# Kernel tuning notes

Hardware: AMD Instinct MI355X
Metric: run time of the kernel (lower is better)

## Reference

```python
import jax, jax.numpy as jnp
import numpy as np

EPS = 1e-5
D_MODEL = 128; D_INNER = 256; D_STATE = 64; D_CONV = 4; NHEADS = 8; HEADDIM = 32
N_LAYERS = 4; PATCH = 16; IMG = 512; BATCH = 16
D_IN_PROJ = 2 * D_INNER + 2 * D_STATE + NHEADS  # 648
CONV_DIM = D_INNER + 2 * D_STATE               # 384


def _layernorm(x, g, b):
    m = jnp.mean(x, -1, keepdims=True)
    v = jnp.mean((x - m) ** 2, -1, keepdims=True)
    return (x - m) * jax.lax.rsqrt(v + EPS) * g + b


def _mamba2(x, in_w, conv_w, conv_b, dt_bias, A_log, D_skip, norm_w, out_w):
    # x: (b, l, d_model). Faithful to mamba-ssm Mamba2 (ngroups=1, rmsnorm gated, D skip).
    b, l, _ = x.shape
    zxbcdt = jnp.einsum('bld,ed->ble', x, in_w)            # (b,l,648)
    z = zxbcdt[..., :D_INNER]
    xBC = zxbcdt[..., D_INNER:D_INNER + CONV_DIM]
    dt = zxbcdt[..., -NHEADS:]
    # causal depthwise conv1d (kernel D_CONV) + SiLU
    xpad = jnp.pad(xBC, ((0, 0), (D_CONV - 1, 0), (0, 0)))
    xc = conv_b + sum(xpad[:, k:k + l, :] * conv_w[:, k] for k in range(D_CONV))
    xc = jax.nn.silu(xc)
    xs = xc[..., :D_INNER]
    B = xc[..., D_INNER:D_INNER + D_STATE]                 # (b,l,n)
    C = xc[..., -D_STATE:]                                 # (b,l,n)
    dt = jax.nn.softplus(dt + dt_bias)                     # (b,l,h)
    dA = jnp.exp(dt * (-jnp.exp(A_log)))                   # (b,l,h)
    xh = xs.reshape(b, l, NHEADS, HEADDIM)                 # (b,l,h,p)

    def step(hstate, t):
        dA_t, dt_t, B_t, x_t, C_t = t
        hstate = hstate * dA_t[:, :, None, None] + jnp.einsum('bh,bn,bhp->bhpn', dt_t, B_t, x_t)
        return hstate, jnp.einsum('bhpn,bn->bhp', hstate, C_t)

    h0 = jnp.zeros((b, NHEADS, HEADDIM, D_STATE), x.dtype)
    _, ys = jax.lax.scan(step, h0, (dA.swapaxes(0, 1), dt.swapaxes(0, 1), B.swapaxes(0, 1), xh.swapaxes(0, 1), C.swapaxes(0, 1)))
    y = ys.swapaxes(0, 1) + D_skip[None, None, :, None] * xh
    y = y.reshape(b, l, D_INNER)
    y = y * jax.nn.silu(z)                                 # gate
    y = y * jax.lax.rsqrt(jnp.mean(y * y, -1, keepdims=True) + EPS) * norm_w  # gated RMSNorm
    return jnp.einsum('ble,de->bld', y, out_w)


def _forward(x, patch_w, patch_b, pe_g, pe_b, in_w, conv_w, conv_b, dt_bias, A_log,
             D_skip, ssm_norm_w, out_w, ln_g, ln_b, fn_g, fn_b, attn_w1, attn_b1, attn_w2, attn_b2):
    b = x.shape[0]
    Hp = x.shape[2] // PATCH; Wp = x.shape[3] // PATCH
    # patch-embed conv (stride==kernel) as a reshape + einsum
    xp = x.reshape(b, 3, Hp, PATCH, Wp, PATCH)
    tok = jnp.einsum('bchpwq,dcpq->bhwd', xp, patch_w) + patch_b
    tok = tok.reshape(b, Hp * Wp, D_MODEL)
    tok = _layernorm(tok, pe_g, pe_b)
    for i in range(N_LAYERS):
        res = tok
        tok = _layernorm(tok, ln_g[i], ln_b[i])
        tok = _mamba2(tok, in_w[i], conv_w[i], conv_b[i], dt_bias[i], A_log[i],
                      D_skip[i], ssm_norm_w[i], out_w[i])
        tok = tok + res
    tok = _layernorm(tok, fn_g, fn_b)
    # attention pooling
    h1 = jnp.tanh(jnp.einsum('bld,hd->blh', tok, attn_w1) + attn_b1)
    scores = jnp.einsum('blh,oh->blo', h1, attn_w2) + attn_b2
    w = jax.nn.softmax(scores, axis=1)
    pooled = jnp.sum(w * tok, axis=1)
    nrm = jnp.maximum(jnp.sqrt(jnp.sum(pooled * pooled, -1, keepdims=True)), 1e-12)
    return pooled / nrm


def setup_inputs() -> dict:
    key = jax.random.key(0)
    ks = jax.random.split(key, 16)
    n = lambda k, shape, s=0.02: (jax.random.normal(k, shape) * s).astype(jnp.float32)
    return {
        'x': jax.random.normal(ks[0], (BATCH, 3, IMG, IMG), jnp.float32),
        'patch_w': n(ks[1], (D_MODEL, 3, PATCH, PATCH)),
        'patch_b': jnp.zeros((D_MODEL,), jnp.float32),
        'pe_g': jnp.ones((D_MODEL,), jnp.float32),
        'pe_b': jnp.zeros((D_MODEL,), jnp.float32),
        'in_w': n(ks[2], (N_LAYERS, D_IN_PROJ, D_MODEL)),
        'conv_w': n(ks[3], (N_LAYERS, CONV_DIM, D_CONV), 0.1),
        'conv_b': jnp.zeros((N_LAYERS, CONV_DIM), jnp.float32),
        'dt_bias': n(ks[4], (N_LAYERS, NHEADS), 0.5),
        'A_log': jnp.log(jax.random.uniform(ks[5], (N_LAYERS, NHEADS), jnp.float32, 1.0, 16.0)),
        'D_skip': jnp.ones((N_LAYERS, NHEADS), jnp.float32),
        'ssm_norm_w': jnp.ones((N_LAYERS, D_INNER), jnp.float32),
        'out_w': n(ks[6], (N_LAYERS, D_MODEL, D_INNER)),
        'ln_g': jnp.ones((N_LAYERS, D_MODEL), jnp.float32),
        'ln_b': jnp.zeros((N_LAYERS, D_MODEL), jnp.float32),
        'fn_g': jnp.ones((D_MODEL,), jnp.float32),
        'fn_b': jnp.zeros((D_MODEL,), jnp.float32),
        'attn_w1': n(ks[7], (D_MODEL // 2, D_MODEL), 0.05),
        'attn_b1': jnp.zeros((D_MODEL // 2,), jnp.float32),
        'attn_w2': n(ks[8], (1, D_MODEL // 2), 0.05),
        'attn_b2': jnp.zeros((1,), jnp.float32),
    }


def reference(x, patch_w, patch_b, pe_g, pe_b, in_w, conv_w, conv_b, dt_bias, A_log,
              D_skip, ssm_norm_w, out_w, ln_g, ln_b, fn_g, fn_b, attn_w1, attn_b1, attn_w2, attn_b2):
    return _forward(x, patch_w, patch_b, pe_g, pe_b, in_w, conv_w, conv_b, dt_bias, A_log,
                    D_skip, ssm_norm_w, out_w, ln_g, ln_b, fn_g, fn_b, attn_w1, attn_b1, attn_w2, attn_b2)
```

## Files before the change

### kernel.cpp

```cpp
#include <hip/hip_runtime.h>
#include <math.h>

#define EPS 1e-5f

constexpr int NB      = 16;
constexpr int L       = 1024;
constexpr int DM      = 128;
constexpr int DI      = 256;
constexpr int DS      = 64;
constexpr int NH      = 8;
constexpr int DPROJ   = 648;
constexpr int CDIM    = 384;
constexpr int EPAD    = 656;

typedef __attribute__((ext_vector_type(8))) short short8v;
typedef __attribute__((ext_vector_type(4))) short short4v;
typedef __attribute__((ext_vector_type(4))) float f32x4;
typedef unsigned short ushort_t;

__device__ __forceinline__ float silu_f(float x){ return x / (1.f + expf(-x)); }
__device__ __forceinline__ ushort_t f2bf(float f){
  union { float f; unsigned int u; } v; v.f = f;
  unsigned int r = v.u + 0x7FFF + ((v.u >> 16) & 1);
  return (ushort_t)(r >> 16);
}
__device__ __forceinline__ float bf2f(ushort_t u){
  union { float f; unsigned int u; } v; v.u = ((unsigned int)u) << 16;
  return v.f;
}
__device__ __forceinline__ short8v pack8(float4 a, float4 b){
  short8v v;
  v[0]=(short)f2bf(a.x); v[1]=(short)f2bf(a.y); v[2]=(short)f2bf(a.z); v[3]=(short)f2bf(a.w);
  v[4]=(short)f2bf(b.x); v[5]=(short)f2bf(b.y); v[6]=(short)f2bf(b.z); v[7]=(short)f2bf(b.w);
  return v;
}

__global__ __launch_bounds__(256) void k_cvt(const float* __restrict__ in_w,
    const float* __restrict__ ln_g, const float* __restrict__ ln_b,
    const float* __restrict__ out_w, const float* __restrict__ nw,
    const float* __restrict__ patch_w, const float* __restrict__ w1,
    ushort_t* __restrict__ inwb, ushort_t* __restrict__ owb,
    ushort_t* __restrict__ pwb, float* __restrict__ biasin,
    ushort_t* __restrict__ w1b){
  const int R1 = 4 * EPAD * 128, R2 = 4 * 128 * 256, R3 = 128 * 768, R4 = 4 * EPAD, R5 = 64 * 128;
  int i = blockIdx.x * 256 + threadIdx.x;
  if (i < R1) {
    int ly = i / (EPAD * 128), rem = i % (EPAD * 128), e = rem >> 7, d = rem & 127;
    float v = 0.f;
    if (e < DPROJ) v = in_w[((size_t)ly * DPROJ + e) * 128 + d] * ln_g[ly * 128 + d];
    inwb[i] = f2bf(v);
    return;
  }
  i -= R1;
  if (i < R2) {
    int ly = i >> 15, rem = i & 32767, e = rem & 255;
    owb[i] = f2bf(out_w[i] * nw[ly * 256 + e]);
    return;
  }
  i -= R2;
  if (i < R3) { pwb[i] = f2bf(patch_w[i]); return; }
  i -= R3;
  if (i < R4) {
    int ly = i / EPAD, e = i % EPAD;
    float s = 0.f;
    if (e < DPROJ) {
      const float* r = in_w + ((size_t)ly * DPROJ + e) * 128;
      const float* b = ln_b + ly * 128;
      for (int d = 0; d < 128; ++d) s += r[d] * b[d];
    }
    biasin[i] = s;
    return;
  }
  i -= R4;
  if (i < R5) w1b[i] = f2bf(w1[i]);
}

__global__ __launch_bounds__(256) void k_patch(const float* __restrict__ x,
    const ushort_t* __restrict__ pwb, const float* __restrict__ pb,
    const float* __restrict__ pg, const float* __restrict__ pbe,
    float* __restrict__ tok){
  __shared__ ushort_t Al[64 * 128];
  __shared__ ushort_t Bl[128 * 128];
  __shared__ float spb[128], spg[128], spe[128];
  const int m0 = blockIdx.x * 64;
  const int tid = threadIdx.x;
  char* Ab = (char*)Al; char* Bb = (char*)Bl;
  if (tid < 128) { spb[tid] = pb[tid]; spg[tid] = pg[tid]; spe[tid] = pbe[tid]; }
  const int w = tid >> 6, l = tid & 63, lr = l & 15, lgp = l >> 4;
  f32x4 acc[8];
#pragma unroll
  for (int nt = 0; nt < 8; ++nt) acc[nt] = (f32x4){0.f, 0.f, 0.f, 0.f};
  for (int kc = 0; kc < 6; ++kc) {
    __syncthreads();
    for (int idx = tid; idx < 128 * 16; idx += 256) {
      int n = idx >> 4, ch = idx & 15;
      short8v v = *(const short8v*)(pwb + (size_t)n * 768 + kc * 128 + (ch << 3));
      *(short8v*)(Bb + n * 256 + ((ch * 16) ^ ((n & 7) << 4))) = v;
    }
    {
      const int c = kc >> 1;
      for (int i = tid; i < 1024; i += 256) {
        int t = i >> 4, p = (i >> 1) & 7, o = i & 1;
        int T = m0 + t, bb = T >> 10, tl = T & 1023, hp = tl >> 5, wp = tl & 31;
        const float* src = x + (((size_t)(bb * 3 + c) * 512 + hp * 16 + ((kc & 1) << 3) + p) * 512
                                + wp * 16 + o * 8);
        float4 f0 = *(const float4*)src;
        float4 f1 = *(const float4*)(src + 4);
        short8v v = pack8(f0, f1);
        int kk = p * 16 + o * 8;
        *(short8v*)(Ab + t * 256 + ((kk * 2) ^ ((t & 7) << 4))) = v;
      }
    }
    __syncthreads();
    short8v a[4];
#pragma unroll
    for (int ks = 0; ks < 4; ++ks)
      a[ks] = *(const short8v*)(Ab + (16 * w + lr) * 256 + ((ks * 64 + lgp * 16) ^ ((lr & 7) << 4)));
#pragma unroll
    for (int nt = 0; nt < 8; ++nt) {
#pragma unroll
      for (int ks = 0; ks < 4; ++ks) {
        short8v b = *(const short8v*)(Bb + (nt * 16 + lr) * 256 + ((ks * 64 + lgp * 16) ^ ((lr & 7) << 4)));
        acc[nt] = __builtin_amdgcn_mfma_f32_16x16x32_bf16(a[ks], b, acc[nt], 0, 0, 0);
      }
    }
  }
  float s4[4] = {0,0,0,0}, q4[4] = {0,0,0,0};
#pragma unroll
  for (int nt = 0; nt < 8; ++nt) {
    const float bb = spb[nt * 16 + lr];
#pragma unroll
    for (int r = 0; r < 4; ++r) { float v = acc[nt][r] + bb; s4[r] += v; q4[r] += v * v; }
  }
#pragma unroll
  for (int r = 0; r < 4; ++r) {
    for (int off = 1; off < 16; off <<= 1) {
      s4[r] += __shfl_xor(s4[r], off, 16);
      q4[r] += __shfl_xor(q4[r], off, 16);
    }
  }
#pragma unroll
  for (int r = 0; r < 4; ++r) {
    float mean = s4[r] * (1.f / 128.f);
    float var  = q4[r] * (1.f / 128.f) - mean * mean;
    float rstd = rsqrtf(var + EPS);
    const size_t row = (size_t)(m0 + 16 * w + lgp * 4 + r) * 128;
#pragma unroll
    for (int nt = 0; nt < 8; ++nt) {
      int col = nt * 16 + lr;
      float v = acc[nt][r] + spb[col];
      tok[row + col] = (v - mean) * rstd * spg[col] + spe[col];
    }
  }
}

__global__ __launch_bounds__(256) void k_inproj(const float* __restrict__ tok,
    const ushort_t* __restrict__ inwb, const float* __restrict__ biasin,
    float* __restrict__ zx){
  __shared__ ushort_t Al[128 * 128];
  __shared__ ushort_t Bl[176 * 128];
  __shared__ float sBias[176];
  const int blk = blockIdx.x;
  const int mb = blk >> 2, nb = blk & 3;
  const int m0 = mb << 7, n0 = nb * 176;
  const int NT = (nb == 3) ? 128 : 176;
  const int tid = threadIdx.x;
  char* Ab = (char*)Al; char* Bb = (char*)Bl;
  for (int idx = tid; idx < (NT << 4); idx += 256) {
    int row = idx >> 4, ch = idx & 15;
    short8v v = *(const short8v*)(inwb + ((size_t)(n0 + row) << 7) + (ch << 3));
    *(short8v*)(Bb + row * 256 + ((ch * 16) ^ ((row & 7) << 4))) = v;
  }
  for (int idx = tid; idx < NT; idx += 256) sBias[idx] = biasin[n0 + idx];
  for (int rp = 0; rp < 2; ++rp) {
    const int r = (rp << 6) + (tid >> 2), t4 = tid & 3;
    const float* src = tok + (((size_t)(m0 + r)) << 7) + t4 * 32;
    float v[32];
    float s = 0.f, sq = 0.f;
#pragma unroll
    for (int k = 0; k < 8; ++k) {
      float4 f = *(const float4*)(src + 4 * k);
      v[4*k] = f.x; v[4*k+1] = f.y; v[4*k+2] = f.z; v[4*k+3] = f.w;
      s += f.x + f.y + f.z + f.w;
      sq += f.x*f.x + f.y*f.y + f.z*f.z + f.w*f.w;
    }
    s  += __shfl_xor(s, 1, 4);  s  += __shfl_xor(s, 2, 4);
    sq += __shfl_xor(sq, 1, 4); sq += __shfl_xor(sq, 2, 4);
    float mean = s * (1.f / 128.f);
    float var  = sq * (1.f / 128.f) - mean * mean;
    float rstd = rsqrtf(var + EPS);
#pragma unroll
    for (int k = 0; k < 4; ++k) {
      short8v o;
#pragma unroll
      for (int e = 0; e < 8; ++e) o[e] = (short)f2bf((v[8*k + e] - mean) * rstd);
      *(short8v*)(Ab + r * 256 + ((t4 * 64 + 16 * k) ^ ((r & 7) << 4))) = o;
    }
  }
  __syncthreads();
  const int w = tid >> 6, l = tid & 63, lr = l & 15, lgp = l >> 4;
  const int xsl = (lr & 7) << 4;
  short8v a[2][4];
#pragma unroll
  for (int mi = 0; mi < 2; ++mi) {
    const int mt = w + mi * 4;
#pragma unroll
    for (int ks = 0; ks < 4; ++ks)
      a[mi][ks] = *(const short8v*)(Ab + (16 * mt + lr) * 256 + ((ks * 64 + lgp * 16) ^ xsl));
  }
  const int NTT = NT >> 4;
  for (int nt = 0; nt < NTT; ++nt) {
    f32x4 acc0 = (f32x4){0.f, 0.f, 0.f, 0.f};
    f32x4 acc1 = (f32x4){0.f, 0.f, 0.f, 0.f};
#pragma unroll
    for (int ks = 0; ks < 4; ++ks) {
      short8v b = *(const short8v*)(Bb + (nt * 16 + lr) * 256 + ((ks * 64 + lgp * 16) ^ xsl));
      acc0 = __builtin_amdgcn_mfma_f32_16x16x32_bf16(a[0][ks], b, acc0, 0, 0, 0);
      acc1 = __builtin_amdgcn_mfma_f32_16x16x32_bf16(a[1][ks], b, acc1, 0, 0, 0);
    }
    const int col = n0 + nt * 16 + lr;
    if (col < DPROJ) {
      const float bias = sBias[nt * 16 + lr];
#pragma unroll
      for (int r = 0; r < 4; ++r) {
        zx[((size_t)(m0 + 16 * w       + lgp * 4 + r)) * DPROJ + col] = acc0[r] + bias;
        zx[((size_t)(m0 + 16 * (w + 4) + lgp * 4 + r)) * DPROJ + col] = acc1[r] + bias;
      }
    }
  }
}

constexpr int CONVC = 192;
__global__ __launch_bounds__(256) void k_conv(const float* __restrict__ zx,
    const float* __restrict__ cw, const float* __restrict__ cb,
    const float* __restrict__ dtbias, const float* __restrict__ Alog,
    ushort_t* __restrict__ xc, float* __restrict__ dtb,
    float* __restrict__ lcb, float* __restrict__ Acb){
  __shared__ float st[67][CONVC];
  __shared__ float swt[CONVC][4];
  __shared__ float sbias[CONVC];
  const int blk = blockIdx.x;
  const int cg = blk & 1, tile = (blk >> 1) & 15, b = blk >> 5;
  const int l0 = tile << 6, ch0 = cg * CONVC;
  const int tid = threadIdx.x;
  for (int i = tid; i < CONVC; i += 256) {
    float4 wv = *(const float4*)(cw + (size_t)(ch0 + i) * 4);
    swt[i][0] = wv.x; swt[i][1] = wv.y; swt[i][2] = wv.z; swt[i][3] = wv.w;
    sbias[i] = cb[ch0 + i];
  }
  for (int i = tid; i < 67 * 48; i += 256) {
    int rr = i / 48, q4 = i % 48;
    int lrow = l0 + rr - 3;
    float4 v = make_float4(0.f, 0.f, 0.f, 0.f);
    if (lrow >= 0) v = *(const float4*)(zx + ((size_t)(b << 10) + lrow) * DPROJ + DI + ch0 + q4 * 4);
    *(float4*)(&st[rr][q4 * 4]) = v;
  }
  if (cg == 0) {
    const int wv = tid >> 6, lane = tid & 63;
#pragma unroll
    for (int i = 0; i < 2; ++i) {
      const int hh = wv * 2 + i;
      float raw = zx[((size_t)(b << 10) + l0 + lane) * DPROJ + 640 + hh] + dtbias[hh];
      float dt = raw > 20.f ? raw : log1pf(expf(raw));
      float cum = dt * (-expf(Alog[hh]));
      for (int off = 1; off < 64; off <<= 1) {
        float v = __shfl_up(cum, off, 64);
        if (lane >= off) cum += v;
      }
      size_t o = ((size_t)((b << 3) + hh) << 10) + l0 + lane;
      dtb[o] = dt; lcb[o] = cum;
      if (lane == 63) Acb[((b << 3) + hh) * 16 + tile] = expf(cum);
    }
  }
  __syncthreads();
  for (int i = tid; i < 64 * 48; i += 256) {
    int t = i / 48, g = i % 48;
    short4v ov;
#pragma unroll
    for (int j = 0; j < 4; ++j) {
      int c2 = g * 4 + j;
      float acc = sbias[c2] + st[t][c2] * swt[c2][0] + st[t+1][c2] * swt[c2][1]
                + st[t+2][c2] * swt[c2][2] + st[t+3][c2] * swt[c2][3];
      ov[j] = (short)f2bf(silu_f(acc));
    }
    *(short4v*)(xc + ((size_t)(b << 10) + l0 + t) * CDIM + ch0 + g * 4) = ov;
  }
}

__global__ __launch_bounds__(256) void k_cstate(const ushort_t* __restrict__ xc,
    const float* __restrict__ dtb, const float* __restrict__ lcb,
    float* __restrict__ Sc){
  __shared__ ushort_t sXc[32 * 64];
  __shared__ ushort_t sBt[64 * 64];
  __shared__ float scoef[64];
  const int blk = blockIdx.x;
  const int c = blk & 15, h = (blk >> 4) & 7, b = blk >> 7;
  const int tid = threadIdx.x;
  const int l0 = c << 6;
  char* pA = (char*)sXc; char* pB = (char*)sBt;
  const size_t obh = ((size_t)((b << 3) + h) << 10) + l0;
  if (tid < 64) {
    float lcT = lcb[obh + 63];
    scoef[tid] = dtb[obh + tid] * __expf(fminf(lcT - lcb[obh + tid], 0.f));
  }
  const int s = tid >> 2, q = tid & 3;
  const ushort_t* xr = xc + ((size_t)(b << 10) + l0 + s) * CDIM;
  short8v b0 = *(const short8v*)(xr + 256 + q * 16);
  short8v b1 = *(const short8v*)(xr + 256 + q * 16 + 8);
  short8v x8 = *(const short8v*)(xr + (h << 5) + q * 8);
#pragma unroll
  for (int j = 0; j < 16; ++j) {
    const int n = q * 16 + j;
    ushort_t bv = (ushort_t)(j < 8 ? b0[j] : b1[j - 8]);
    *(ushort_t*)(pB + n * 128 + ((s * 2) ^ ((n & 7) << 4))) = bv;
  }
  __syncthreads();
  const float cf = scoef[s];
#pragma unroll
  for (int j = 0; j < 8; ++j) {
    const int p = q * 8 + j;
    *(ushort_t*)(pA + p * 128 + ((s * 2) ^ ((p & 7) << 4))) = f2bf(cf * bf2f((ushort_t)x8[j]));
  }
  __syncthreads();
  const int w = tid >> 6, l = tid & 63, lr = l & 15, lgp = l >> 4;
  const int xsl = (lr & 7) << 4;
  const int pt = w & 1, ng = w >> 1;
  short8v a0 = *(const short8v*)(pA + (pt * 16 + lr) * 128 + ((lgp * 16) ^ xsl));
  short8v a1 = *(const short8v*)(pA + (pt * 16 + lr) * 128 + ((64 + lgp * 16) ^ xsl));
  float* dst = Sc + ((size_t)blk << 11);
#pragma unroll
  for (int ni = 0; ni < 2; ++ni) {
    const int nt = ng * 2 + ni;
    f32x4 acc = (f32x4){0.f, 0.f, 0.f, 0.f};
    short8v bb0 = *(const short8v*)(pB + (nt * 16 + lr) * 128 + ((lgp * 16) ^ xsl));
    short8v bb1 = *(const short8v*)(pB + (nt * 16 + lr) * 128 + ((64 + lgp * 16) ^ xsl));
    acc = __builtin_amdgcn_mfma_f32_16x16x32_bf16(a0, bb0, acc, 0, 0, 0);
    acc = __builtin_amdgcn_mfma_f32_16x16x32_bf16(a1, bb1, acc, 0, 0, 0);
#pragma unroll
    for (int r = 0; r < 4; ++r)
      dst[(pt * 16 + lgp * 4 + r) * 64 + nt * 16 + lr] = acc[r];
  }
}

__global__ __launch_bounds__(256) void k_hscan(float* __restrict__ Sc, const float* __restrict__ Acb){
  const int blk = blockIdx.x;
  const int bh = blk >> 3;
  const int e = ((blk & 7) << 8) + threadIdx.x;
  float hs = 0.f;
  const size_t base = ((size_t)bh << 15) + e;
  for (int c = 0; c < 16; ++c) {
    const size_t o = base + ((size_t)c << 11);
    float v = Sc[o];
    Sc[o] = hs;
    hs = Acb[(bh << 4) + c] * hs + v;
  }
}

__global__ __launch_bounds__(256) void k_chunky(const ushort_t* __restrict__ xc,
    const float* __restrict__ h0buf, const float* __restrict__ dtb,
    const float* __restrict__ lcb, const float* __restrict__ Dsk,
    ushort_t* __restrict__ ys){
  __shared__ ushort_t sC[64 * 64];
  __shared__ ushort_t sBm[64 * 64];
  __shared__ ushort_t sAW[64 * 128];
  __shared__ ushort_t sBX[32 * 128];
  __shared__ float sXT[32][65];
  __shared__ float sdt[64], slc[64];
  const int blk = blockIdx.x;
  const int c = blk & 15, h = (blk >> 4) & 7, b = blk >> 7;
  const int tid = threadIdx.x;
  const int l0 = c << 6;
  char* pC = (char*)sC; char* pB = (char*)sBm; char* pA = (char*)sAW; char* pX = (char*)sBX;
  const size_t obh = ((size_t)((b << 3) + h) << 10) + l0;
  if (tid < 64) { sdt[tid] = dtb[obh + tid]; slc[tid] = lcb[obh + tid]; }
  {
    const int row = tid >> 2, q = tid & 3;
    const ushort_t* xr = xc + ((size_t)(b << 10) + l0 + row) * CDIM;
    const int xs = (row & 7) << 4;
    short8v b0 = *(const short8v*)(xr + 256 + q * 16);
    short8v b1 = *(const short8v*)(xr + 256 + q * 16 + 8);
    *(short8v*)(pB + row * 128 + ((q * 32) ^ xs))      = b0;
    *(short8v*)(pB + row * 128 + ((q * 32 + 16) ^ xs)) = b1;
    short8v c0 = *(const short8v*)(xr + 320 + q * 16);
    short8v c1 = *(const short8v*)(xr + 320 + q * 16 + 8);
    *(short8v*)(pC + row * 128 + ((q * 32) ^ xs))      = c0;
    *(short8v*)(pC + row * 128 + ((q * 32 + 16) ^ xs)) = c1;
    const float Pt = __expf(lcb[obh + row]);
    short8v q0, q1;
#pragma unroll
    for (int j = 0; j < 8; ++j) {
      q0[j] = (short)f2bf(Pt * bf2f((ushort_t)c0[j]));
      q1[j] = (short)f2bf(Pt * bf2f((ushort_t)c1[j]));
    }
    *(short8v*)(pA + row * 256 + ((128 + q * 32) ^ xs))      = q0;
    *(short8v*)(pA + row * 256 + ((128 + q * 32 + 16) ^ xs)) = q1;
    short8v x8 = *(const short8v*)(xr + (h << 5) + q * 8);
#pragma unroll
    for (int j = 0; j < 8; ++j) sXT[q * 8 + j][row] = bf2f((ushort_t)x8[j]);
  }
  {
    const int p = tid >> 3, n8 = (tid & 7) << 3;
    float4 h0a = *(const float4*)(h0buf + ((size_t)blk << 11) + (p << 6) + n8);
    float4 h0b = *(const float4*)(h0buf + ((size_t)blk << 11) + (p << 6) + n8 + 4);
    *(short8v*)(pX + p * 256 + (((64 + n8) * 2) ^ ((p & 7) << 4))) = pack8(h0a, h0b);
  }
  __syncthreads();
  {
    const int p = tid >> 3, s8 = (tid & 7) << 3;
    short8v vx;
#pragma unroll
    for (int e = 0; e < 8; ++e) vx[e] = (short)f2bf(sXT[p][s8 + e]);
    *(short8v*)(pX + p * 256 + ((s8 * 2) ^ ((p & 7) << 4))) = vx;
  }
  const int w = tid >> 6, l = tid & 63, lr = l & 15, lgp = l >> 4;
  const int xsl = (lr & 7) << 4;
  f32x4 accg[4];
#pragma unroll
  for (int nt = 0; nt < 4; ++nt) accg[nt] = (f32x4){0.f, 0.f, 0.f, 0.f};
  {
    short8v a0 = *(const short8v*)(pC + (16 * w + lr) * 128 + ((lgp * 16) ^ xsl));
    short8v a1 = *(const short8v*)(pC + (16 * w + lr) * 128 + ((64 + lgp * 16) ^ xsl));
#pragma unroll
    for (int nt = 0; nt < 4; ++nt) {
      short8v b0 = *(const short8v*)(pB + (nt * 16 + lr) * 128 + ((lgp * 16) ^ xsl));
      short8v b1 = *(const short8v*)(pB + (nt * 16 + lr) * 128 + ((64 + lgp * 16) ^ xsl));
      accg[nt] = __builtin_amdgcn_mfma_f32_16x16x32_bf16(a0, b0, accg[nt], 0, 0, 0);
      accg[nt] = __builtin_amdgcn_mfma_f32_16x16x32_bf16(a1, b1, accg[nt], 0, 0, 0);
    }
  }
#pragma unroll
  for (int nt = 0; nt < 4; ++nt) {
    const int s = nt * 16 + lr;
    const float ds = sdt[s], ls = slc[s];
#pragma unroll
    for (int r = 0; r < 4; ++r) {
      const int t = 16 * w + lgp * 4 + r;
      float wv = 0.f;
      if (s <= t) wv = ds * __expf(fminf(slc[t] - ls, 0.f)) * accg[nt][r];
      *(ushort_t*)(pA + t * 256 + ((s * 2) ^ ((t & 7) << 4))) = f2bf(wv);
    }
  }
  __syncthreads();
  f32x4 accy[2];
  accy[0] = (f32x4){0.f, 0.f, 0.f, 0.f};
  accy[1] = (f32x4){0.f, 0.f, 0.f, 0.f};
  short8v aw[4];
#pragma unroll
  for (int ks = 0; ks < 4; ++ks)
    aw[ks] = *(const short8v*)(pA + (16 * w + lr) * 256 + ((ks * 64 + lgp * 16) ^ xsl));
#pragma unroll
  for (int nt = 0; nt < 2; ++nt) {
#pragma unroll
    for (int ks = 0; ks < 4; ++ks) {
      short8v bx = *(const short8v*)(pX + (nt * 16 + lr) * 256 + ((ks * 64 + lgp * 16) ^ xsl));
      accy[nt] = __builtin_amdgcn_mfma_f32_16x16x32_bf16(aw[ks], bx, accy[nt], 0, 0, 0);
    }
  }
  const float dsk = Dsk[h];
#pragma unroll
  for (int nt = 0; nt < 2; ++nt) {
    const int p = nt * 16 + lr;
#pragma unroll
    for (int r = 0; r < 4; ++r) {
      const int t = 16 * w + lgp * 4 + r;
      ys[((size_t)(b << 10) + l0 + t) * DI + (h << 5) + p] = f2bf(accy[nt][r] + dsk * sXT[p][t]);
    }
  }
}

__global__ __launch_bounds__(256) void k_gateout(const float* __restrict__ zx,
    const ushort_t* __restrict__ ysb, const ushort_t* __restrict__ owb,
    float* __restrict__ tok){
  __shared__ ushort_t Al[64 * 256];
  __shared__ ushort_t Bl[128 * 64];
  const int m0 = blockIdx.x * 64;
  const int tid = threadIdx.x;
  char* Ab = (char*)Al; char* Bb = (char*)Bl;
  {
    const int r = tid >> 2, t4 = tid & 3;
    const size_t row = (size_t)(m0 + r);
    const ushort_t* yp = ysb + row * 256 + t4 * 64;
    const float* zp = zx + row * DPROJ + t4 * 64;
    float p[64];
    float sq = 0.f;
#pragma unroll
    for (int k = 0; k < 8; ++k) {
      short8v y8 = *(const short8v*)(yp + 8 * k);
      float4 fz0 = *(const float4*)(zp + 8 * k);
      float4 fz1 = *(const float4*)(zp + 8 * k + 4);
      float zz[8] = {fz0.x, fz0.y, fz0.z, fz0.w, fz1.x, fz1.y, fz1.z, fz1.w};
#pragma unroll
      for (int j = 0; j < 8; ++j) {
        float a = bf2f((ushort_t)y8[j]) * (zz[j] / (1.f + __expf(-zz[j])));
        p[8 * k + j] = a; sq += a * a;
      }
    }
    sq += __shfl_xor(sq, 1, 4); sq += __shfl_xor(sq, 2, 4);
    float rstd = rsqrtf(sq * (1.f / 256.f) + EPS);
#pragma unroll
    for (int k = 0; k < 8; ++k) {
      short8v o;
#pragma unroll
      for (int e = 0; e < 8; ++e) o[e] = (short)f2bf(p[8*k + e] * rstd);
      *(short8v*)(Ab + r * 512 + ((t4 * 128 + 16 * k) ^ ((r & 7) << 4))) = o;
    }
  }
  const int w = tid >> 6, l = tid & 63, lr = l & 15, lgp = l >> 4;
  f32x4 acc[8];
#pragma unroll
  for (int nt = 0; nt < 8; ++nt) acc[nt] = (f32x4){0.f, 0.f, 0.f, 0.f};
  for (int kq = 0; kq < 4; ++kq) {
    __syncthreads();
    for (int idx = tid; idx < 128 * 8; idx += 256) {
      int row = idx >> 3, ch = idx & 7;
      short8v v = *(const short8v*)(owb + ((size_t)row << 8) + kq * 64 + (ch << 3));
      *(short8v*)(Bb + row * 128 + ((ch * 16) ^ ((row & 7) << 4))) = v;
    }
    __syncthreads();
    short8v a0 = *(const short8v*)(Ab + (16*w + lr) * 512 + ((kq * 128 +      lgp * 16) ^ ((lr & 7) << 4)));
    short8v a1 = *(const short8v*)(Ab + (16*w + lr) * 512 + ((kq * 128 + 64 + lgp * 16) ^ ((lr & 7) << 4)));
#pragma unroll
    for (int nt = 0; nt < 8; ++nt) {
      short8v b0 = *(const short8v*)(Bb + (nt * 16 + lr) * 128 + ((     lgp * 16) ^ ((lr & 7) << 4)));
      short8v b1 = *(const short8v*)(Bb + (nt * 16 + lr) * 128 + ((64 + lgp * 16) ^ ((lr & 7) << 4)));
      acc[nt] = __builtin_amdgcn_mfma_f32_16x16x32_bf16(a0, b0, acc[nt], 0, 0, 0);
      acc[nt] = __builtin_amdgcn_mfma_f32_16x16x32_bf16(a1, b1, acc[nt], 0, 0, 0);
    }
  }
#pragma unroll
  for (int nt = 0; nt < 8; ++nt) {
#pragma unroll
    for (int r = 0; r < 4; ++r) {
      tok[((size_t)(m0 + 16 * w + lgp * 4 + r)) * 128 + nt * 16 + lr] += acc[nt][r];
    }
  }
}

__global__ __launch_bounds__(256) void k_score(const float* __restrict__ tok,
    const float* __restrict__ fg, const float* __restrict__ fb,
    const ushort_t* __restrict__ w1b, const float* __restrict__ b1,
    const float* __restrict__ w2, const float* __restrict__ b2,
    float* __restrict__ tokF, float* __restrict__ sc){
  __shared__ ushort_t Al[64 * 128];
  __shared__ ushort_t Wl[64 * 128];
  __shared__ float sb1[64], sw2[64];
  const int m0 = blockIdx.x * 64;
  const int tid = threadIdx.x;
  char* Ab = (char*)Al; char* Wb = (char*)Wl;
  for (int idx = tid; idx < 64 * 16; idx += 256) {
    int row = idx >> 4, ch = idx & 15;
    short8v v = *(const short8v*)(w1b + (row << 7) + (ch << 3));
    *(short8v*)(Wb + row * 256 + ((ch * 16) ^ ((row & 7) << 4))) = v;
  }
  if (tid < 64) { sb1[tid] = b1[tid]; sw2[tid] = w2[tid]; }
  {
    const int r = tid >> 2, t4 = tid & 3;
    const float* src = tok + (((size_t)(m0 + r)) << 7) + t4 * 32;
    float v[32];
    float s = 0.f, sq = 0.f;
#pragma unroll
    for (int k = 0; k < 8; ++k) {
      float4 f = *(const float4*)(src + 4 * k);
      v[4*k] = f.x; v[4*k+1] = f.y; v[4*k+2] = f.z; v[4*k+3] = f.w;
      s += f.x + f.y + f.z + f.w;
      sq += f.x*f.x + f.y*f.y + f.z*f.z + f.w*f.w;
    }
    s  += __shfl_xor(s, 1, 4);  s  += __shfl_xor(s, 2, 4);
    sq += __shfl_xor(sq, 1, 4); sq += __shfl_xor(sq, 2, 4);
    float mean = s * (1.f / 128.f);
    float var  = sq * (1.f / 128.f) - mean * mean;
    float rstd = rsqrtf(var + EPS);
    float* tdst = tokF + (((size_t)(m0 + r)) << 7) + t4 * 32;
#pragma unroll
    for (int k = 0; k < 4; ++k) {
      float o8[8];
      float4 g0 = *(const float4*)(fg + t4 * 32 + 8 * k);
      float4 g1 = *(const float4*)(fg + t4 * 32 + 8 * k + 4);
      float4 e0 = *(const float4*)(fb + t4 * 32 + 8 * k);
      float4 e1 = *(const float4*)(fb + t4 * 32 + 8 * k + 4);
      o8[0] = (v[8*k+0]-mean)*rstd*g0.x + e0.x; o8[1] = (v[8*k+1]-mean)*rstd*g0.y + e0.y;
      o8[2] = (v[8*k+2]-mean)*rstd*g0.z + e0.z; o8[3] = (v[8*k+3]-mean)*rstd*g0.w + e0.w;
      o8[4] = (v[8*k+4]-mean)*rstd*g1.x + e1.x; o8[5] = (v[8*k+5]-mean)*rstd*g1.y + e1.y;
      o8[6] = (v[8*k+6]-mean)*rstd*g1.z + e1.z; o8[7] = (v[8*k+7]-mean)*rstd*g1.w + e1.w;
      *(float4*)(tdst + 8*k)     = make_float4(o8[0], o8[1], o8[2], o8[3]);
      *(float4*)(tdst + 8*k + 4) = make_float4(o8[4], o8[5], o8[6], o8[7]);
      short8v ov;
#pragma unroll
      for (int e = 0; e < 8; ++e) ov[e] = (short)f2bf(o8[e]);
      *(short8v*)(Ab + r * 256 + ((t4 * 64 + 16 * k) ^ ((r & 7) << 4))) = ov;
    }
  }
  __syncthreads();
  const int w = tid >> 6, l = tid & 63, lr = l & 15, lgp = l >> 4;
  const int xsl = (lr & 7) << 4;
  short8v a[4];
#pragma unroll
  for (int ks = 0; ks < 4; ++ks)
    a[ks] = *(const short8v*)(Ab + (16 * w + lr) * 256 + ((ks * 64 + lgp * 16) ^ xsl));
  float sacc[4] = {0.f, 0.f, 0.f, 0.f};
#pragma unroll
  for (int nt = 0; nt < 4; ++nt) {
    f32x4 acc = (f32x4){0.f, 0.f, 0.f, 0.f};
#pragma unroll
    for (int ks = 0; ks < 4; ++ks) {
      short8v bb = *(const short8v*)(Wb + (nt * 16 + lr) * 256 + ((ks * 64 + lgp * 16) ^ xsl));
      acc = __builtin_amdgcn_mfma_f32_16x16x32_bf16(a[ks], bb, acc, 0, 0, 0);
    }
    const float bias = sb1[nt * 16 + lr], wv = sw2[nt * 16 + lr];
#pragma unroll
    for (int r = 0; r < 4; ++r) sacc[r] += tanhf(acc[r] + bias) * wv;
  }
#pragma unroll
  for (int r = 0; r < 4; ++r) {
    for (int off = 1; off < 16; off <<= 1) sacc[r] += __shfl_xor(sacc[r], off, 16);
  }
  if (lr == 0) {
    const float bb2 = b2[0];
#pragma unroll
    for (int r = 0; r < 4; ++r) sc[m0 + 16 * w + lgp * 4 + r] = sacc[r] + bb2;
  }
}

__global__ __launch_bounds__(256) void k_pool1(const float* __restrict__ tokF,
    const float* __restrict__ sc, float* __restrict__ pp){
  __shared__ float sw[128];
  __shared__ float sacc[128];
  __shared__ float sse[2];
  const int bs = blockIdx.x, b = bs >> 3, seg = bs & 7, tid = threadIdx.x;
  const int l0 = (b << 10) + (seg << 7);
  if (tid < 128) sw[tid] = __expf(sc[l0 + tid]);
  __syncthreads();
  const int d = tid & 127, g = tid >> 7;
  const float* tf = tokF + ((size_t)(l0 + (g << 6))) * 128 + d;
  float acc = 0.f;
#pragma unroll 4
  for (int i = 0; i < 64; ++i) acc += sw[(g << 6) + i] * tf[(size_t)i * 128];
  if (g == 0) sacc[d] = acc;
  float e = (tid < 128) ? sw[tid] : 0.f;
  for (int off = 32; off; off >>= 1) e += __shfl_xor(e, off);
  if ((tid & 63) == 0 && tid < 128) sse[tid >> 6] = e;
  __syncthreads();
  if (g == 1) pp[bs * 132 + d] = sacc[d] + acc;
  if (tid == 0) pp[bs * 132 + 128] = sse[0] + sse[1];
}

__global__ __launch_bounds__(128) void k_pool2(const float* __restrict__ pp,
    float* __restrict__ out){
  __shared__ float s2[2];
  const int b = blockIdx.x, tid = threadIdx.x;
  float num = 0.f, den = 0.f;
#pragma unroll
  for (int seg = 0; seg < 8; ++seg) {
    num += pp[(b * 8 + seg) * 132 + tid];
    den += pp[(b * 8 + seg) * 132 + 128];
  }
  float pooled = num / den;
  float sq = pooled * pooled;
  for (int off = 32; off; off >>= 1) sq += __shfl_xor(sq, off);
  if ((tid & 63) == 0) s2[tid >> 6] = sq;
  __syncthreads();
  float nrm = fmaxf(sqrtf(s2[0] + s2[1]), 1e-12f);
  out[(size_t)b * 128 + tid] = pooled / nrm;
}

extern "C" void kernel_launch(void* const* d_in, const int* in_sizes, int n_in,
                              void* d_out, int out_size, void* d_ws, size_t ws_size,
                              hipStream_t stream) {
  const float* x       = (const float*)d_in[0];
  const float* patch_w = (const float*)d_in[1];
  const float* patch_b = (const float*)d_in[2];
  const float* pe_g    = (const float*)d_in[3];
  const float* pe_b    = (const float*)d_in[4];
  const float* in_w    = (const float*)d_in[5];
  const float* conv_w  = (const float*)d_in[6];
  const float* conv_b  = (const float*)d_in[7];
  const float* dt_bias = (const float*)d_in[8];
  const float* A_log   = (const float*)d_in[9];
  const float* D_skip  = (const float*)d_in[10];
  const float* nw      = (const float*)d_in[11];
  const float* out_w   = (const float*)d_in[12];
  const float* ln_g    = (const float*)d_in[13];
  const float* ln_b    = (const float*)d_in[14];
  const float* fn_g    = (const float*)d_in[15];
  const float* fn_b    = (const float*)d_in[16];
  const float* w1      = (const float*)d_in[17];
  const float* b1      = (const float*)d_in[18];
  const float* w2      = (const float*)d_in[19];
  const float* b2      = (const float*)d_in[20];
  float* out = (float*)d_out;
  char* ws = (char*)d_ws;

  size_t off = 0;
  float* tok  = (float*)(ws + off); off += (size_t)NB * L * DM * 4;
  float* zx   = (float*)(ws + off); off += (size_t)NB * L * DPROJ * 4;
  ushort_t* xcb = (ushort_t*)(ws + off); off += (size_t)NB * L * CDIM * 2;
  ushort_t* ysb = (ushort_t*)(ws + off); off += (size_t)NB * L * DI * 2;
  float* Scb  = (float*)(ws + off); off += (size_t)NB * NH * 16 * 2048 * 4;
  float* dtb  = (float*)(ws + off); off += (size_t)NB * NH * L * 4;
  float* lcb  = (float*)(ws + off); off += (size_t)NB * NH * L * 4;
  float* Acb  = (float*)(ws + off); off += (size_t)NB * NH * 16 * 4;
  ushort_t* inwb = (ushort_t*)(ws + off); off += (size_t)4 * EPAD * 128 * 2;
  ushort_t* owb  = (ushort_t*)(ws + off); off += (size_t)4 * 128 * 256 * 2;
  ushort_t* pwb  = (ushort_t*)(ws + off); off += (size_t)128 * 768 * 2;
  float* biasin  = (float*)(ws + off); off += (size_t)4 * EPAD * 4;
  ushort_t* w1b  = (ushort_t*)(ws + off); off += (size_t)64 * 128 * 2;
  float* pp      = (float*)(ws + off); off += (size_t)128 * 132 * 4;
  float* tokF = zx;
  float* scb  = (float*)(ws + (size_t)30 * 1024 * 1024);

  {
    const int total = 4 * EPAD * 128 + 4 * 128 * 256 + 128 * 768 + 4 * EPAD + 64 * 128;
    k_cvt<<<(total + 255) / 256, 256, 0, stream>>>(in_w, ln_g, ln_b, out_w, nw, patch_w, w1,
                                                   inwb, owb, pwb, biasin, w1b);
  }
  k_patch<<<256, 256, 0, stream>>>(x, pwb, patch_b, pe_g, pe_b, tok);
  for (int ly = 0; ly < 4; ++ly) {
    k_inproj<<<512, 256, 0, stream>>>(tok, inwb + (size_t)ly * EPAD * 128,
                                      biasin + ly * EPAD, zx);
    k_conv<<<NB * 16 * 2, 256, 0, stream>>>(zx, conv_w + (size_t)ly * CDIM * 4,
                                            conv_b + ly * CDIM, dt_bias + ly * NH,
                                            A_log + ly * NH, xcb, dtb, lcb, Acb);
    k_cstate<<<NB * NH * 16, 256, 0, stream>>>(xcb, dtb, lcb, Scb);
    k_hscan<<<NB * NH * 8, 256, 0, stream>>>(Scb, Acb);
    k_chunky<<<NB * NH * 16, 256, 0, stream>>>(xcb, Scb, dtb, lcb,
                                               D_skip + ly * NH, ysb);
    k_gateout<<<256, 256, 0, stream>>>(zx, ysb, owb + (size_t)ly * 128 * 256, tok);
  }
  k_score<<<256, 256, 0, stream>>>(tok, fn_g, fn_b, w1b, b1, w2, b2, tokF, scb);
  k_pool1<<<128, 256, 0, stream>>>(tokF, scb, pp);
  k_pool2<<<16, 128, 0, stream>>>(pp, out);
}
```

Baseline: 478.5 us.

## Store in-proj output and chunk states in bf16, prefetch out-proj weights

Switches the large zx intermediate (in-projection output) and the per-chunk SSM state buffer from fp32 to bf16. This halves global memory traffic across inproj, conv, hscan, chunky and gateout. In gateout, the out-projection weight tiles are now prefetched into registers and staged through double-buffered shared memory, which removes one barrier per k-step. The cost is lower precision, including in the inter-chunk state recurrence that hscan runs in bf16 storage. The tokF and scb workspace offsets are moved to fit the new layout.

After: 430.1 us. 1.11x faster.

```diff
diff --git a/kernel.cpp b/kernel.cpp
--- a/kernel.cpp
+++ b/kernel.cpp
@@ -156,7 +156,7 @@
 
 __global__ __launch_bounds__(256) void k_inproj(const float* __restrict__ tok,
     const ushort_t* __restrict__ inwb, const float* __restrict__ biasin,
-    float* __restrict__ zx){
+    ushort_t* __restrict__ zxb){
   __shared__ ushort_t Al[128 * 128];
   __shared__ ushort_t Bl[176 * 128];
   __shared__ float sBias[176];
@@ -223,15 +223,15 @@
       const float bias = sBias[nt * 16 + lr];
 #pragma unroll
       for (int r = 0; r < 4; ++r) {
-        zx[((size_t)(m0 + 16 * w       + lgp * 4 + r)) * DPROJ + col] = acc0[r] + bias;
-        zx[((size_t)(m0 + 16 * (w + 4) + lgp * 4 + r)) * DPROJ + col] = acc1[r] + bias;
+        zxb[((size_t)(m0 + 16 * w       + lgp * 4 + r)) * DPROJ + col] = f2bf(acc0[r] + bias);
+        zxb[((size_t)(m0 + 16 * (w + 4) + lgp * 4 + r)) * DPROJ + col] = f2bf(acc1[r] + bias);
       }
     }
   }
 }
 
 constexpr int CONVC = 192;
-__global__ __launch_bounds__(256) void k_conv(const float* __restrict__ zx,
+__global__ __launch_bounds__(256) void k_conv(const ushort_t* __restrict__ zxb,
     const float* __restrict__ cw, const float* __restrict__ cb,
     const float* __restrict__ dtbias, const float* __restrict__ Alog,
     ushort_t* __restrict__ xc, float* __restrict__ dtb,
@@ -248,19 +248,24 @@
     swt[i][0] = wv.x; swt[i][1] = wv.y; swt[i][2] = wv.z; swt[i][3] = wv.w;
     sbias[i] = cb[ch0 + i];
   }
-  for (int i = tid; i < 67 * 48; i += 256) {
-    int rr = i / 48, q4 = i % 48;
+  for (int i = tid; i < 67 * 24; i += 256) {
+    int rr = i / 24, g = i % 24;
     int lrow = l0 + rr - 3;
-    float4 v = make_float4(0.f, 0.f, 0.f, 0.f);
-    if (lrow >= 0) v = *(const float4*)(zx + ((size_t)(b << 10) + lrow) * DPROJ + DI + ch0 + q4 * 4);
-    *(float4*)(&st[rr][q4 * 4]) = v;
+    float v[8] = {0,0,0,0,0,0,0,0};
+    if (lrow >= 0) {
+      short8v z8 = *(const short8v*)(zxb + ((size_t)(b << 10) + lrow) * DPROJ + DI + ch0 + g * 8);
+#pragma unroll
+      for (int j = 0; j < 8; ++j) v[j] = bf2f((ushort_t)z8[j]);
+    }
+    *(float4*)(&st[rr][g * 8])     = make_float4(v[0], v[1], v[2], v[3]);
+    *(float4*)(&st[rr][g * 8 + 4]) = make_float4(v[4], v[5], v[6], v[7]);
   }
   if (cg == 0) {
     const int wv = tid >> 6, lane = tid & 63;
 #pragma unroll
     for (int i = 0; i < 2; ++i) {
       const int hh = wv * 2 + i;
-      float raw = zx[((size_t)(b << 10) + l0 + lane) * DPROJ + 640 + hh] + dtbias[hh];
+      float raw = bf2f(zxb[((size_t)(b << 10) + l0 + lane) * DPROJ + 640 + hh]) + dtbias[hh];
       float dt = raw > 20.f ? raw : log1pf(expf(raw));
       float cum = dt * (-expf(Alog[hh]));
       for (int off = 1; off < 64; off <<= 1) {
@@ -289,7 +294,7 @@
 
 __global__ __launch_bounds__(256) void k_cstate(const ushort_t* __restrict__ xc,
     const float* __restrict__ dtb, const float* __restrict__ lcb,
-    float* __restrict__ Sc){
+    ushort_t* __restrict__ Sc){
   __shared__ ushort_t sXc[32 * 64];
   __shared__ ushort_t sBt[64 * 64];
   __shared__ float scoef[64];
@@ -327,7 +332,7 @@
   const int pt = w & 1, ng = w >> 1;
   short8v a0 = *(const short8v*)(pA + (pt * 16 + lr) * 128 + ((lgp * 16) ^ xsl));
   short8v a1 = *(const short8v*)(pA + (pt * 16 + lr) * 128 + ((64 + lgp * 16) ^ xsl));
-  float* dst = Sc + ((size_t)blk << 11);
+  ushort_t* dst = Sc + ((size_t)blk << 11);
 #pragma unroll
   for (int ni = 0; ni < 2; ++ni) {
     const int nt = ng * 2 + ni;
@@ -338,11 +343,11 @@
     acc = __builtin_amdgcn_mfma_f32_16x16x32_bf16(a1, bb1, acc, 0, 0, 0);
 #pragma unroll
     for (int r = 0; r < 4; ++r)
-      dst[(pt * 16 + lgp * 4 + r) * 64 + nt * 16 + lr] = acc[r];
-  }
-}
-
-__global__ __launch_bounds__(256) void k_hscan(float* __restrict__ Sc, const float* __restrict__ Acb){
+      dst[(pt * 16 + lgp * 4 + r) * 64 + nt * 16 + lr] = f2bf(acc[r]);
+  }
+}
+
+__global__ __launch_bounds__(256) void k_hscan(ushort_t* __restrict__ Sc, const float* __restrict__ Acb){
   const int blk = blockIdx.x;
   const int bh = blk >> 3;
   const int e = ((blk & 7) << 8) + threadIdx.x;
@@ -350,14 +355,14 @@
   const size_t base = ((size_t)bh << 15) + e;
   for (int c = 0; c < 16; ++c) {
     const size_t o = base + ((size_t)c << 11);
-    float v = Sc[o];
-    Sc[o] = hs;
+    float v = bf2f(Sc[o]);
+    Sc[o] = f2bf(hs);
     hs = Acb[(bh << 4) + c] * hs + v;
   }
 }
 
 __global__ __launch_bounds__(256) void k_chunky(const ushort_t* __restrict__ xc,
-    const float* __restrict__ h0buf, const float* __restrict__ dtb,
+    const ushort_t* __restrict__ h0buf, const float* __restrict__ dtb,
     const float* __restrict__ lcb, const float* __restrict__ Dsk,
     ushort_t* __restrict__ ys){
   __shared__ ushort_t sC[64 * 64];
@@ -400,9 +405,8 @@
   }
   {
     const int p = tid >> 3, n8 = (tid & 7) << 3;
-    float4 h0a = *(const float4*)(h0buf + ((size_t)blk << 11) + (p << 6) + n8);
-    float4 h0b = *(const float4*)(h0buf + ((size_t)blk << 11) + (p << 6) + n8 + 4);
-    *(short8v*)(pX + p * 256 + (((64 + n8) * 2) ^ ((p & 7) << 4))) = pack8(h0a, h0b);
+    short8v h8 = *(const short8v*)(h0buf + ((size_t)blk << 11) + (p << 6) + n8);
+    *(short8v*)(pX + p * 256 + (((64 + n8) * 2) ^ ((p & 7) << 4))) = h8;
   }
   __syncthreads();
   {
@@ -468,30 +472,29 @@
   }
 }
 
-__global__ __launch_bounds__(256) void k_gateout(const float* __restrict__ zx,
+__global__ __launch_bounds__(256) void k_gateout(const ushort_t* __restrict__ zxb,
     const ushort_t* __restrict__ ysb, const ushort_t* __restrict__ owb,
     float* __restrict__ tok){
   __shared__ ushort_t Al[64 * 256];
-  __shared__ ushort_t Bl[128 * 64];
+  __shared__ ushort_t Bl[2][128 * 64];
   const int m0 = blockIdx.x * 64;
   const int tid = threadIdx.x;
-  char* Ab = (char*)Al; char* Bb = (char*)Bl;
+  char* Ab = (char*)Al;
   {
     const int r = tid >> 2, t4 = tid & 3;
     const size_t row = (size_t)(m0 + r);
     const ushort_t* yp = ysb + row * 256 + t4 * 64;
-    const float* zp = zx + row * DPROJ + t4 * 64;
+    const ushort_t* zp = zxb + row * DPROJ + t4 * 64;
     float p[64];
     float sq = 0.f;
 #pragma unroll
     for (int k = 0; k < 8; ++k) {
       short8v y8 = *(const short8v*)(yp + 8 * k);
-      float4 fz0 = *(const float4*)(zp + 8 * k);
-      float4 fz1 = *(const float4*)(zp + 8 * k + 4);
-      float zz[8] = {fz0.x, fz0.y, fz0.z, fz0.w, fz1.x, fz1.y, fz1.z, fz1.w};
+      short8v z8 = *(const short8v*)(zp + 8 * k);
 #pragma unroll
       for (int j = 0; j < 8; ++j) {
-        float a = bf2f((ushort_t)y8[j]) * (zz[j] / (1.f + __expf(-zz[j])));
+        float zz = bf2f((ushort_t)z8[j]);
+        float a = bf2f((ushort_t)y8[j]) * (zz / (1.f + __expf(-zz)));
         p[8 * k + j] = a; sq += a * a;
       }
     }
@@ -505,18 +508,32 @@
       *(short8v*)(Ab + r * 512 + ((t4 * 128 + 16 * k) ^ ((r & 7) << 4))) = o;
     }
   }
+  short8v breg[4];
+#pragma unroll
+  for (int j = 0; j < 4; ++j) {
+    int idx = tid + 256 * j, row = idx >> 3, ch = idx & 7;
+    breg[j] = *(const short8v*)(owb + ((size_t)row << 8) + (ch << 3));
+  }
   const int w = tid >> 6, l = tid & 63, lr = l & 15, lgp = l >> 4;
   f32x4 acc[8];
 #pragma unroll
   for (int nt = 0; nt < 8; ++nt) acc[nt] = (f32x4){0.f, 0.f, 0.f, 0.f};
+  int buf = 0;
   for (int kq = 0; kq < 4; ++kq) {
+    char* Bb = (char*)Bl[buf];
+#pragma unroll
+    for (int j = 0; j < 4; ++j) {
+      int idx = tid + 256 * j, row = idx >> 3, ch = idx & 7;
+      *(short8v*)(Bb + row * 128 + ((ch * 16) ^ ((row & 7) << 4))) = breg[j];
+    }
     __syncthreads();
-    for (int idx = tid; idx < 128 * 8; idx += 256) {
-      int row = idx >> 3, ch = idx & 7;
-      short8v v = *(const short8v*)(owb + ((size_t)row << 8) + kq * 64 + (ch << 3));
-      *(short8v*)(Bb + row * 128 + ((ch * 16) ^ ((row & 7) << 4))) = v;
-    }
-    __syncthreads();
+    if (kq < 3) {
+#pragma unroll
+      for (int j = 0; j < 4; ++j) {
+        int idx = tid + 256 * j, row = idx >> 3, ch = idx & 7;
+        breg[j] = *(const short8v*)(owb + ((size_t)row << 8) + (kq + 1) * 64 + (ch << 3));
+      }
+    }
     short8v a0 = *(const short8v*)(Ab + (16*w + lr) * 512 + ((kq * 128 +      lgp * 16) ^ ((lr & 7) << 4)));
     short8v a1 = *(const short8v*)(Ab + (16*w + lr) * 512 + ((kq * 128 + 64 + lgp * 16) ^ ((lr & 7) << 4)));
 #pragma unroll
@@ -526,6 +543,7 @@
       acc[nt] = __builtin_amdgcn_mfma_f32_16x16x32_bf16(a0, b0, acc[nt], 0, 0, 0);
       acc[nt] = __builtin_amdgcn_mfma_f32_16x16x32_bf16(a1, b1, acc[nt], 0, 0, 0);
     }
+    buf ^= 1;
   }
 #pragma unroll
   for (int nt = 0; nt < 8; ++nt) {
@@ -692,10 +710,10 @@
 
   size_t off = 0;
   float* tok  = (float*)(ws + off); off += (size_t)NB * L * DM * 4;
-  float* zx   = (float*)(ws + off); off += (size_t)NB * L * DPROJ * 4;
+  ushort_t* zxb = (ushort_t*)(ws + off); off += (size_t)NB * L * DPROJ * 2;
   ushort_t* xcb = (ushort_t*)(ws + off); off += (size_t)NB * L * CDIM * 2;
   ushort_t* ysb = (ushort_t*)(ws + off); off += (size_t)NB * L * DI * 2;
-  float* Scb  = (float*)(ws + off); off += (size_t)NB * NH * 16 * 2048 * 4;
+  ushort_t* Scb = (ushort_t*)(ws + off); off += (size_t)NB * NH * 16 * 2048 * 2;
   float* dtb  = (float*)(ws + off); off += (size_t)NB * NH * L * 4;
   float* lcb  = (float*)(ws + off); off += (size_t)NB * NH * L * 4;
   float* Acb  = (float*)(ws + off); off += (size_t)NB * NH * 16 * 4;
@@ -705,8 +723,8 @@
   float* biasin  = (float*)(ws + off); off += (size_t)4 * EPAD * 4;
   ushort_t* w1b  = (ushort_t*)(ws + off); off += (size_t)64 * 128 * 2;
   float* pp      = (float*)(ws + off); off += (size_t)128 * 132 * 4;
-  float* tokF = zx;
-  float* scb  = (float*)(ws + (size_t)30 * 1024 * 1024);
+  float* tokF = (float*)(ws + (size_t)8 * 1024 * 1024);
+  float* scb  = (float*)(ws + (size_t)17 * 1024 * 1024);
 
   {
     const int total = 4 * EPAD * 128 + 4 * 128 * 256 + 128 * 768 + 4 * EPAD + 64 * 128;
@@ -716,15 +734,15 @@
   k_patch<<<256, 256, 0, stream>>>(x, pwb, patch_b, pe_g, pe_b, tok);
   for (int ly = 0; ly < 4; ++ly) {
     k_inproj<<<512, 256, 0, stream>>>(tok, inwb + (size_t)ly * EPAD * 128,
-                                      biasin + ly * EPAD, zx);
-    k_conv<<<NB * 16 * 2, 256, 0, stream>>>(zx, conv_w + (size_t)ly * CDIM * 4,
+                                      biasin + ly * EPAD, zxb);
+    k_conv<<<NB * 16 * 2, 256, 0, stream>>>(zxb, conv_w + (size_t)ly * CDIM * 4,
                                             conv_b + ly * CDIM, dt_bias + ly * NH,
                                             A_log + ly * NH, xcb, dtb, lcb, Acb);
     k_cstate<<<NB * NH * 16, 256, 0, stream>>>(xcb, dtb, lcb, Scb);
     k_hscan<<<NB * NH * 8, 256, 0, stream>>>(Scb, Acb);
     k_chunky<<<NB * NH * 16, 256, 0, stream>>>(xcb, Scb, dtb, lcb,
                                                D_skip + ly * NH, ysb);
-    k_gateout<<<256, 256, 0, stream>>>(zx, ysb, owb + (size_t)ly * 128 * 256, tok);
+    k_gateout<<<256, 256, 0, stream>>>(zxb, ysb, owb + (size_t)ly * 128 * 256, tok);
   }
   k_score<<<256, 256, 0, stream>>>(tok, fn_g, fn_b, w1b, b1, w2, b2, tokF, scb);
   k_pool1<<<128, 256, 0, stream>>>(tokF, scb, pp);
```
